# Performance work log

Hardware: AMD Instinct MI355X
Metric: run time of the kernel (lower is better)

## Reference

```python
import jax, jax.numpy as jnp
import numpy as np

N, E = 50000, 800000
IN_DIM, HID_DIM, OUT_DIM = 512, 256, 128


def setup_inputs() -> dict:
    key = jax.random.key(0)
    ks = jax.random.split(key, 10)
    x = jax.random.normal(ks[0], (N, IN_DIM), dtype=jnp.float32)
    edge_index = jax.random.randint(ks[1], (2, E), 0, N, dtype=jnp.int64)
    edge_weight = jax.random.uniform(ks[2], (E,), dtype=jnp.float32)
    # GCNConv weights (PyG stores weight as [in, out]; out = x @ W + b)
    def glorot(k, fan_in, fan_out):
        lim = np.sqrt(6.0 / (fan_in + fan_out)).astype(np.float32)
        return jax.random.uniform(k, (fan_in, fan_out), minval=-lim, maxval=lim, dtype=jnp.float32)
    W1 = glorot(ks[3], IN_DIM, HID_DIM)
    b1 = jnp.zeros((HID_DIM,), dtype=jnp.float32)
    W2 = glorot(ks[4], HID_DIM, OUT_DIM)
    b2 = jnp.zeros((OUT_DIM,), dtype=jnp.float32)
    Wp = glorot(ks[5], OUT_DIM, OUT_DIM)
    bp = jnp.zeros((OUT_DIM,), dtype=jnp.float32)
    return {"x": x, "edge_index": edge_index, "edge_weight": edge_weight,
            "W1": W1, "b1": b1, "W2": W2, "b2": b2, "Wp": Wp, "bp": bp}


def _gcn_norm(edge_index, edge_weight, n_nodes):
    # add self loops with weight 1.0 (PyG gcn_norm, fill_value=1.0)
    loops = jnp.arange(n_nodes, dtype=edge_index.dtype)
    row = jnp.concatenate([edge_index[0], loops])
    col = jnp.concatenate([edge_index[1], loops])
    w = jnp.concatenate([edge_weight, jnp.ones((n_nodes,), edge_weight.dtype)])
    deg = jax.ops.segment_sum(w, col, num_segments=n_nodes)  # [N]
    dinv = jnp.where(deg > 0, jax.lax.rsqrt(deg), 0.0)
    norm = dinv[row] * w * dinv[col]  # [E+N]
    return row, col, norm


def _gcn_conv(h, row, col, norm, W, b, n_nodes):
    h = h @ W                              # [N, out]
    msgs = h[row] * norm[:, None]          # gather + scale  [E+N, out]
    out = jax.ops.segment_sum(msgs, col, num_segments=n_nodes)  # scatter-add
    return out + b


def reference(x, edge_index, edge_weight, W1, b1, W2, b2, Wp, bp):
    n_nodes = x.shape[0]
    # eval mode: F.dropout(edge_weight, training=False) is identity
    row, col, norm = _gcn_norm(edge_index, edge_weight, n_nodes)
    h = jax.nn.relu(_gcn_conv(x, row, col, norm, W1, b1, n_nodes))
    # eval mode: F.dropout identity
    h = _gcn_conv(h, row, col, norm, W2, b2, n_nodes)
    return h @ Wp + bp
```

## Files before the change

kernel.cpp:

```cpp
#include <hip/hip_runtime.h>

#define IN_DIM 512
#define HID_DIM 256
#define OUT_DIM 128
#define BCAP 64

typedef unsigned short u16;
typedef __attribute__((ext_vector_type(8))) short bf16x8;
typedef __attribute__((ext_vector_type(4))) float f32x4;

__device__ inline u16 f2bf(float f) {
    unsigned u = __float_as_uint(f);
    return (u16)((u + 0x7FFFu + ((u >> 16) & 1u)) >> 16);
}
__device__ inline float bf2f(u16 u) {
    return __uint_as_float(((unsigned)u) << 16);
}

__device__ inline void gld_lds16(const void* g, void* l) {
    __builtin_amdgcn_global_load_lds((const __attribute__((address_space(1))) unsigned*)g,
                                     (__attribute__((address_space(3))) unsigned*)l, 16, 0, 0);
}


__global__ void bucket_fill_kernel(const int* __restrict__ row, const int* __restrict__ col,
                                   const float* __restrict__ w,
                                   int* __restrict__ cnt, int2* __restrict__ bucket, int E) {
    int e = blockIdx.x * blockDim.x + threadIdx.x;
    if (e >= E) return;
    int c = col[e];
    int slot = atomicAdd(&cnt[c], 1);
    if (slot < BCAP) {
        int2 v;
        v.x = row[e];
        v.y = __float_as_int(w[e]);
        bucket[(size_t)c * BCAP + slot] = v;
    }
}

__global__ void deg_dinv_kernel(const int2* __restrict__ bucket, const int* __restrict__ cnt,
                                float* __restrict__ dinv, int n) {
    int i = blockIdx.x * blockDim.x + threadIdx.x;
    if (i >= n) return;
    int c = min(cnt[i], BCAP);
    const int2* b = bucket + (size_t)i * BCAP;
    float s = 1.0f;
    for (int p = 0; p < c; ++p) s += __int_as_float(b[p].y);
    dinv[i] = (s > 0.0f) ? rsqrtf(s) : 0.0f;
}


__global__ void convert_x_kernel(const float* __restrict__ X, u16* __restrict__ Xb,
                                 int M, int Mpad) {
    long tid = (long)blockIdx.x * blockDim.x + threadIdx.x;
    long total = (long)Mpad * IN_DIM / 8;
    if (tid >= total) return;
    long base = tid * 8;
    int r = (int)(base / IN_DIM);
    ushort4 lo, hi;
    if (r < M) {
        float4 f0 = *(const float4*)(X + base);
        float4 f1 = *(const float4*)(X + base + 4);
        lo.x = f2bf(f0.x); lo.y = f2bf(f0.y); lo.z = f2bf(f0.z); lo.w = f2bf(f0.w);
        hi.x = f2bf(f1.x); hi.y = f2bf(f1.y); hi.z = f2bf(f1.z); hi.w = f2bf(f1.w);
    } else {
        lo.x = lo.y = lo.z = lo.w = 0;
        hi.x = hi.y = hi.z = hi.w = 0;
    }
    *(ushort4*)(Xb + base) = lo;
    *(ushort4*)(Xb + base + 4) = hi;
}

__global__ void transpose_bf_kernel(const float* __restrict__ W, u16* __restrict__ WT,
                                    int K, int Nc) {
    int idx = blockIdx.x * blockDim.x + threadIdx.x;
    if (idx >= K * Nc) return;
    int nrow = idx / K, k = idx - nrow * K;
    WT[idx] = f2bf(W[(size_t)k * Nc + nrow]);
}

__global__ void fuse_w2p_kernel(const float* __restrict__ W2, const float* __restrict__ Wp,
                                u16* __restrict__ W2pT) {
    int idx = blockIdx.x * blockDim.x + threadIdx.x;
    if (idx >= OUT_DIM * HID_DIM) return;
    int n = idx / HID_DIM, k = idx - n * HID_DIM;
    float s = 0.0f;
    for (int m = 0; m < OUT_DIM; ++m)
        s = fmaf(W2[(size_t)k * OUT_DIM + m], Wp[(size_t)m * OUT_DIM + n], s);
    W2pT[idx] = f2bf(s);
}

__global__ void fuse_bias2_kernel(const float* __restrict__ b2, const float* __restrict__ Wp,
                                  const float* __restrict__ bp, float* __restrict__ bias2) {
    int n = blockIdx.x * blockDim.x + threadIdx.x;
    if (n >= OUT_DIM) return;
    float s = bp[n];
    for (int m = 0; m < OUT_DIM; ++m)
        s = fmaf(b2[m], Wp[(size_t)m * OUT_DIM + n], s);
    bias2[n] = s;
}


#define TM 128
#define TN 128
#define TK 32

template <typename OutT>
__global__ __launch_bounds__(256)
void mfma_gemm_kernel(const u16* __restrict__ A, const u16* __restrict__ BT,
                      const float* __restrict__ bias, OutT* __restrict__ C,
                      int M, int Nc, int K) {
    __shared__ u16 As[TM * TK];
    __shared__ u16 Bs[TN * TK];
    const int tid = threadIdx.x;
    const int w = tid >> 6, l = tid & 63;
    const int wr = w >> 1, wc = w & 1;
    const long tile_m = (long)blockIdx.x * TM;
    const int tile_n = blockIdx.y * TN;

    const int r0 = w * 32 + (l >> 2);
    const int r1 = r0 + 16;
    const int c0 = l & 3;
    const long ga0 = (tile_m + r0) * (long)K + (long)((c0 ^ (r0 & 3)) * 8);
    const long ga1 = (tile_m + r1) * (long)K + (long)((c0 ^ (r1 & 3)) * 8);
    const long gb0 = (long)(tile_n + r0) * K + (long)((c0 ^ (r0 & 3)) * 8);
    const long gb1 = (long)(tile_n + r1) * K + (long)((c0 ^ (r1 & 3)) * 8);
    u16* ldsA0 = &As[(w * 2 + 0) * 512];
    u16* ldsA1 = &As[(w * 2 + 1) * 512];
    u16* ldsB0 = &Bs[(w * 2 + 0) * 512];
    u16* ldsB1 = &Bs[(w * 2 + 1) * 512];

    f32x4 acc[4][4] = {};
    const int lr = l & 15;
    const int kl = l >> 4;

    for (int k0 = 0; k0 < K; k0 += TK) {
        if (k0) __syncthreads();
        gld_lds16(A + ga0 + k0, ldsA0);
        gld_lds16(A + ga1 + k0, ldsA1);
        gld_lds16(BT + gb0 + k0, ldsB0);
        gld_lds16(BT + gb1 + k0, ldsB1);
        __syncthreads();

        bf16x8 af[4], bfv[4];
#pragma unroll
        for (int mi = 0; mi < 4; ++mi) {
            int rowi = wr * 64 + mi * 16 + lr;
            int byte = rowi * 64 + ((kl ^ (rowi & 3)) * 16);
            af[mi] = *(const bf16x8*)((const char*)As + byte);
        }
#pragma unroll
        for (int ni = 0; ni < 4; ++ni) {
            int rowi = wc * 64 + ni * 16 + lr;
            int byte = rowi * 64 + ((kl ^ (rowi & 3)) * 16);
            bfv[ni] = *(const bf16x8*)((const char*)Bs + byte);
        }
#pragma unroll
        for (int mi = 0; mi < 4; ++mi)
#pragma unroll
            for (int ni = 0; ni < 4; ++ni)
                acc[mi][ni] = __builtin_amdgcn_mfma_f32_16x16x32_bf16(af[mi], bfv[ni], acc[mi][ni], 0, 0, 0);
    }

    float bv[4];
#pragma unroll
    for (int ni = 0; ni < 4; ++ni)
        bv[ni] = bias ? bias[tile_n + wc * 64 + ni * 16 + lr] : 0.0f;
#pragma unroll
    for (int mi = 0; mi < 4; ++mi) {
#pragma unroll
        for (int reg = 0; reg < 4; ++reg) {
            long rowg = tile_m + wr * 64 + mi * 16 + kl * 4 + reg;
            if (rowg < M) {
#pragma unroll
                for (int ni = 0; ni < 4; ++ni) {
                    int colc = tile_n + wc * 64 + ni * 16 + lr;
                    float v = acc[mi][ni][reg] + bv[ni];
                    if constexpr (sizeof(OutT) == 2) C[rowg * Nc + colc] = f2bf(v);
                    else                             C[rowg * Nc + colc] = v;
                }
            }
        }
    }
}


template <int DIM, bool RELU, typename OutT>
__global__ __launch_bounds__(256)
void aggregate_kernel(const u16* __restrict__ t,
                      const int2* __restrict__ bucket,
                      const int* __restrict__ cnt,
                      const float* __restrict__ dinv,
                      const float* __restrict__ bias,
                      OutT* __restrict__ outp, int n) {
    constexpr int V = DIM / 64;
    const int wv = threadIdx.x >> 6;
    const int l = threadIdx.x & 63;
    const int node = blockIdx.x * 4 + wv;
    if (node >= n) return;
    const float dv = dinv[node];
    const float dv2 = dv * dv;
    float acc[V];
    if constexpr (V == 4) {
        ushort4 q = *(const ushort4*)(t + (size_t)node * DIM + l * 4);
        acc[0] = dv2 * bf2f(q.x); acc[1] = dv2 * bf2f(q.y);
        acc[2] = dv2 * bf2f(q.z); acc[3] = dv2 * bf2f(q.w);
    } else {
        ushort2 q = *(const ushort2*)(t + (size_t)node * DIM + l * 2);
        acc[0] = dv2 * bf2f(q.x); acc[1] = dv2 * bf2f(q.y);
    }
    const int e = min(cnt[node], BCAP);
    const int2* b = bucket + (size_t)node * BCAP;
    int p = 0;
    for (; p + 8 <= e; p += 8) {
        int2 ed[8];
        float wt[8];
#pragma unroll
        for (int j = 0; j < 8; ++j) ed[j] = b[p + j];
#pragma unroll
        for (int j = 0; j < 8; ++j) wt[j] = dv * __int_as_float(ed[j].y) * dinv[ed[j].x];
        if constexpr (V == 4) {
            ushort4 q[8];
#pragma unroll
            for (int j = 0; j < 8; ++j) q[j] = *(const ushort4*)(t + (size_t)ed[j].x * DIM + l * 4);
#pragma unroll
            for (int j = 0; j < 8; ++j) {
                acc[0] = fmaf(wt[j], bf2f(q[j].x), acc[0]);
                acc[1] = fmaf(wt[j], bf2f(q[j].y), acc[1]);
                acc[2] = fmaf(wt[j], bf2f(q[j].z), acc[2]);
                acc[3] = fmaf(wt[j], bf2f(q[j].w), acc[3]);
            }
        } else {
            ushort2 q[8];
#pragma unroll
            for (int j = 0; j < 8; ++j) q[j] = *(const ushort2*)(t + (size_t)ed[j].x * DIM + l * 2);
#pragma unroll
            for (int j = 0; j < 8; ++j) {
                acc[0] = fmaf(wt[j], bf2f(q[j].x), acc[0]);
                acc[1] = fmaf(wt[j], bf2f(q[j].y), acc[1]);
            }
        }
    }
    for (; p + 4 <= e; p += 4) {
        int2 ed[4];
        float wt[4];
#pragma unroll
        for (int j = 0; j < 4; ++j) ed[j] = b[p + j];
#pragma unroll
        for (int j = 0; j < 4; ++j) wt[j] = dv * __int_as_float(ed[j].y) * dinv[ed[j].x];
        if constexpr (V == 4) {
            ushort4 q[4];
#pragma unroll
            for (int j = 0; j < 4; ++j) q[j] = *(const ushort4*)(t + (size_t)ed[j].x * DIM + l * 4);
#pragma unroll
            for (int j = 0; j < 4; ++j) {
                acc[0] = fmaf(wt[j], bf2f(q[j].x), acc[0]);
                acc[1] = fmaf(wt[j], bf2f(q[j].y), acc[1]);
                acc[2] = fmaf(wt[j], bf2f(q[j].z), acc[2]);
                acc[3] = fmaf(wt[j], bf2f(q[j].w), acc[3]);
            }
        } else {
            ushort2 q[4];
#pragma unroll
            for (int j = 0; j < 4; ++j) q[j] = *(const ushort2*)(t + (size_t)ed[j].x * DIM + l * 2);
#pragma unroll
            for (int j = 0; j < 4; ++j) {
                acc[0] = fmaf(wt[j], bf2f(q[j].x), acc[0]);
                acc[1] = fmaf(wt[j], bf2f(q[j].y), acc[1]);
            }
        }
    }
    for (; p < e; ++p) {
        int2 e0 = b[p];
        float wgt = dv * __int_as_float(e0.y) * dinv[e0.x];
        if constexpr (V == 4) {
            ushort4 q = *(const ushort4*)(t + (size_t)e0.x * DIM + l * 4);
            acc[0] = fmaf(wgt, bf2f(q.x), acc[0]); acc[1] = fmaf(wgt, bf2f(q.y), acc[1]);
            acc[2] = fmaf(wgt, bf2f(q.z), acc[2]); acc[3] = fmaf(wgt, bf2f(q.w), acc[3]);
        } else {
            ushort2 q = *(const ushort2*)(t + (size_t)e0.x * DIM + l * 2);
            acc[0] = fmaf(wgt, bf2f(q.x), acc[0]); acc[1] = fmaf(wgt, bf2f(q.y), acc[1]);
        }
    }
#pragma unroll
    for (int j = 0; j < V; ++j) {
        float v = acc[j] + bias[l * V + j];
        if (RELU) v = fmaxf(v, 0.0f);
        acc[j] = v;
    }
    if constexpr (sizeof(OutT) == 2) {
        if constexpr (V == 4) {
            ushort4 st;
            st.x = f2bf(acc[0]); st.y = f2bf(acc[1]); st.z = f2bf(acc[2]); st.w = f2bf(acc[3]);
            *(ushort4*)((u16*)outp + (size_t)node * DIM + l * 4) = st;
        } else {
            ushort2 st;
            st.x = f2bf(acc[0]); st.y = f2bf(acc[1]);
            *(ushort2*)((u16*)outp + (size_t)node * DIM + l * 2) = st;
        }
    } else {
        if constexpr (V == 4) {
            float4 st = {acc[0], acc[1], acc[2], acc[3]};
            *(float4*)((float*)outp + (size_t)node * DIM + l * 4) = st;
        } else {
            float2 st = {acc[0], acc[1]};
            *(float2*)((float*)outp + (size_t)node * DIM + l * 2) = st;
        }
    }
}


extern "C" void kernel_launch(void* const* d_in, const int* in_sizes, int n_in,
                              void* d_out, int out_size, void* d_ws, size_t ws_size,
                              hipStream_t stream) {
    const float* x  = (const float*)d_in[0];
    const int*   ei = (const int*)d_in[1];
    const float* ew = (const float*)d_in[2];
    const float* W1 = (const float*)d_in[3];
    const float* b1 = (const float*)d_in[4];
    const float* W2 = (const float*)d_in[5];
    const float* b2 = (const float*)d_in[6];
    const float* Wp = (const float*)d_in[7];
    const float* bp = (const float*)d_in[8];
    float* out = (float*)d_out;

    const int E = in_sizes[2];
    const int N = in_sizes[0] / IN_DIM;
    const int Mpad = ((N + TM - 1) / TM) * TM;
    const int* row = ei;
    const int* col = ei + E;

    size_t off = 0;
    auto carve = [&](size_t bytes) -> void* {
        void* p = (char*)d_ws + off;
        off += (bytes + 255) & ~(size_t)255;
        return p;
    };
    float* dinv   = (float*)carve((size_t)N * 4);
    int*   cnt    = (int*)carve((size_t)N * 4);
    int2*  bucket = (int2*)carve((size_t)N * BCAP * 8);
    u16*   W1T    = (u16*)carve((size_t)HID_DIM * IN_DIM * 2);
    u16*   W2pT   = (u16*)carve((size_t)OUT_DIM * HID_DIM * 2);
    float* bias2  = (float*)carve((size_t)OUT_DIM * 4);
    u16*   bufA   = (u16*)carve((size_t)Mpad * IN_DIM * 2);
    u16*   bufB   = (u16*)carve((size_t)Mpad * HID_DIM * 2);

    u16* x_bf = bufA;
    u16* t1   = bufB;
    u16* a1   = bufA;
    u16* t3   = bufB;

    const int TB = 256;
    const int gN = (N + TB - 1) / TB;
    const int gE = (E + TB - 1) / TB;

    hipMemsetAsync(cnt, 0, (size_t)N * 4, stream);
    bucket_fill_kernel<<<gE, TB, 0, stream>>>(row, col, ew, cnt, bucket, E);
    deg_dinv_kernel<<<gN, TB, 0, stream>>>(bucket, cnt, dinv, N);

    convert_x_kernel<<<(int)(((long)Mpad * IN_DIM / 8 + TB - 1) / TB), TB, 0, stream>>>(x, x_bf, N, Mpad);
    transpose_bf_kernel<<<(IN_DIM * HID_DIM + TB - 1) / TB, TB, 0, stream>>>(W1, W1T, IN_DIM, HID_DIM);
    fuse_w2p_kernel<<<(OUT_DIM * HID_DIM + TB - 1) / TB, TB, 0, stream>>>(W2, Wp, W2pT);
    fuse_bias2_kernel<<<1, OUT_DIM, 0, stream>>>(b2, Wp, bp, bias2);

    const int gm = Mpad / TM;
    const int gagg = (N + 3) / 4;

    mfma_gemm_kernel<u16><<<dim3(gm, HID_DIM / TN), 256, 0, stream>>>(x_bf, W1T, nullptr, t1, Mpad, HID_DIM, IN_DIM);
    aggregate_kernel<HID_DIM, true, u16><<<gagg, 256, 0, stream>>>(t1, bucket, cnt, dinv, b1, a1, N);
    mfma_gemm_kernel<u16><<<dim3(gm, OUT_DIM / TN), 256, 0, stream>>>(a1, W2pT, nullptr, t3, Mpad, OUT_DIM, HID_DIM);
    aggregate_kernel<OUT_DIM, false, float><<<gagg, 256, 0, stream>>>(t3, bucket, cnt, dinv, bias2, out, N);
}
```

Measured before the change: 391.0 us.

## Fuse fp32-to-bf16 conversion of x into first GEMM and merge weight prep kernels

The first GEMM now reads fp32 x directly, converts it to bf16 in registers and writes it into LDS with the same XOR swizzle, masking rows past N. This removes the separate convert pass that wrote and re-read a padded bf16 copy of x. The three small weight and bias prep kernels are merged into one launch to cut launch overhead. The tradeoff is that the A-tile load goes from direct global-to-LDS copies to register-staged loads with conversion ALU work, which could slow the main loop.

Measured after the change: 370.3 us. 1.06x faster.

```diff
diff --git a/kernel.cpp b/kernel.cpp
--- a/kernel.cpp
+++ b/kernel.cpp
@@ -50,54 +50,37 @@
 }
 
 
-__global__ void convert_x_kernel(const float* __restrict__ X, u16* __restrict__ Xb,
-                                 int M, int Mpad) {
-    long tid = (long)blockIdx.x * blockDim.x + threadIdx.x;
-    long total = (long)Mpad * IN_DIM / 8;
-    if (tid >= total) return;
-    long base = tid * 8;
-    int r = (int)(base / IN_DIM);
-    ushort4 lo, hi;
-    if (r < M) {
-        float4 f0 = *(const float4*)(X + base);
-        float4 f1 = *(const float4*)(X + base + 4);
-        lo.x = f2bf(f0.x); lo.y = f2bf(f0.y); lo.z = f2bf(f0.z); lo.w = f2bf(f0.w);
-        hi.x = f2bf(f1.x); hi.y = f2bf(f1.y); hi.z = f2bf(f1.z); hi.w = f2bf(f1.w);
-    } else {
-        lo.x = lo.y = lo.z = lo.w = 0;
-        hi.x = hi.y = hi.z = hi.w = 0;
-    }
-    *(ushort4*)(Xb + base) = lo;
-    *(ushort4*)(Xb + base + 4) = hi;
-}
-
-__global__ void transpose_bf_kernel(const float* __restrict__ W, u16* __restrict__ WT,
-                                    int K, int Nc) {
-    int idx = blockIdx.x * blockDim.x + threadIdx.x;
-    if (idx >= K * Nc) return;
-    int nrow = idx / K, k = idx - nrow * K;
-    WT[idx] = f2bf(W[(size_t)k * Nc + nrow]);
-}
-
-__global__ void fuse_w2p_kernel(const float* __restrict__ W2, const float* __restrict__ Wp,
-                                u16* __restrict__ W2pT) {
-    int idx = blockIdx.x * blockDim.x + threadIdx.x;
-    if (idx >= OUT_DIM * HID_DIM) return;
-    int n = idx / HID_DIM, k = idx - n * HID_DIM;
-    float s = 0.0f;
-    for (int m = 0; m < OUT_DIM; ++m)
-        s = fmaf(W2[(size_t)k * OUT_DIM + m], Wp[(size_t)m * OUT_DIM + n], s);
-    W2pT[idx] = f2bf(s);
-}
-
-__global__ void fuse_bias2_kernel(const float* __restrict__ b2, const float* __restrict__ Wp,
-                                  const float* __restrict__ bp, float* __restrict__ bias2) {
-    int n = blockIdx.x * blockDim.x + threadIdx.x;
-    if (n >= OUT_DIM) return;
-    float s = bp[n];
-    for (int m = 0; m < OUT_DIM; ++m)
-        s = fmaf(b2[m], Wp[(size_t)m * OUT_DIM + n], s);
-    bias2[n] = s;
+__global__ __launch_bounds__(256)
+void weight_prep_kernel(const float* __restrict__ W1, u16* __restrict__ W1T,
+                        const float* __restrict__ W2, const float* __restrict__ Wp,
+                        const float* __restrict__ b2, const float* __restrict__ bp,
+                        u16* __restrict__ W2pT, float* __restrict__ bias2,
+                        int nW1, int nW2p) {
+    const int b = blockIdx.x;
+    const int tid = threadIdx.x;
+    if (b < nW1) {
+        int idx = b * 256 + tid;
+        if (idx >= IN_DIM * HID_DIM) return;
+        int nrow = idx / IN_DIM, k = idx - nrow * IN_DIM;
+        W1T[idx] = f2bf(W1[(size_t)k * HID_DIM + nrow]);
+        return;
+    }
+    if (b < nW1 + nW2p) {
+        int idx = (b - nW1) * 256 + tid;
+        if (idx >= OUT_DIM * HID_DIM) return;
+        int n = idx / HID_DIM, k = idx - n * HID_DIM;
+        float s = 0.0f;
+        for (int m = 0; m < OUT_DIM; ++m)
+            s = fmaf(W2[(size_t)k * OUT_DIM + m], Wp[(size_t)m * OUT_DIM + n], s);
+        W2pT[idx] = f2bf(s);
+        return;
+    }
+    if (tid < OUT_DIM) {
+        float s = bp[tid];
+        for (int m = 0; m < OUT_DIM; ++m)
+            s = fmaf(b2[m], Wp[(size_t)m * OUT_DIM + tid], s);
+        bias2[tid] = s;
+    }
 }
 
 
@@ -105,11 +88,11 @@
 #define TN 128
 #define TK 32
 
-template <typename OutT>
+template <typename AT, typename OutT>
 __global__ __launch_bounds__(256)
-void mfma_gemm_kernel(const u16* __restrict__ A, const u16* __restrict__ BT,
+void mfma_gemm_kernel(const AT* __restrict__ A, const u16* __restrict__ BT,
                       const float* __restrict__ bias, OutT* __restrict__ C,
-                      int M, int Nc, int K) {
+                      int Mreal, int Mpad, int Nc, int K) {
     __shared__ u16 As[TM * TK];
     __shared__ u16 Bs[TN * TK];
     const int tid = threadIdx.x;
@@ -121,14 +104,21 @@
     const int r0 = w * 32 + (l >> 2);
     const int r1 = r0 + 16;
     const int c0 = l & 3;
+    const long gb0 = (long)(tile_n + r0) * K + (long)((c0 ^ (r0 & 3)) * 8);
+    const long gb1 = (long)(tile_n + r1) * K + (long)((c0 ^ (r1 & 3)) * 8);
+    u16* ldsB0 = &Bs[(w * 2 + 0) * 512];
+    u16* ldsB1 = &Bs[(w * 2 + 1) * 512];
+
     const long ga0 = (tile_m + r0) * (long)K + (long)((c0 ^ (r0 & 3)) * 8);
     const long ga1 = (tile_m + r1) * (long)K + (long)((c0 ^ (r1 & 3)) * 8);
-    const long gb0 = (long)(tile_n + r0) * K + (long)((c0 ^ (r0 & 3)) * 8);
-    const long gb1 = (long)(tile_n + r1) * K + (long)((c0 ^ (r1 & 3)) * 8);
     u16* ldsA0 = &As[(w * 2 + 0) * 512];
     u16* ldsA1 = &As[(w * 2 + 1) * 512];
-    u16* ldsB0 = &Bs[(w * 2 + 0) * 512];
-    u16* ldsB1 = &Bs[(w * 2 + 1) * 512];
+
+    const int ci0 = tid, ci1 = tid + 256;
+    const int arow0 = ci0 >> 2, ach0 = ci0 & 3;
+    const int arow1 = ci1 >> 2, ach1 = ci1 & 3;
+    const int ag0 = (ach0 ^ (arow0 & 3)) * 8;
+    const int ag1 = (ach1 ^ (arow1 & 3)) * 8;
 
     f32x4 acc[4][4] = {};
     const int lr = l & 15;
@@ -136,8 +126,31 @@
 
     for (int k0 = 0; k0 < K; k0 += TK) {
         if (k0) __syncthreads();
-        gld_lds16(A + ga0 + k0, ldsA0);
-        gld_lds16(A + ga1 + k0, ldsA1);
+        if constexpr (sizeof(AT) == 4) {
+            float4 f0a = {0,0,0,0}, f0b = {0,0,0,0}, f1a = {0,0,0,0}, f1b = {0,0,0,0};
+            if (tile_m + arow0 < Mreal) {
+                const float* s0 = (const float*)A + (tile_m + arow0) * (long)K + k0 + ag0;
+                f0a = *(const float4*)s0; f0b = *(const float4*)(s0 + 4);
+            }
+            if (tile_m + arow1 < Mreal) {
+                const float* s1 = (const float*)A + (tile_m + arow1) * (long)K + k0 + ag1;
+                f1a = *(const float4*)s1; f1b = *(const float4*)(s1 + 4);
+            }
+            int4 w0, w1;
+            w0.x = f2bf(f0a.x) | ((unsigned)f2bf(f0a.y) << 16);
+            w0.y = f2bf(f0a.z) | ((unsigned)f2bf(f0a.w) << 16);
+            w0.z = f2bf(f0b.x) | ((unsigned)f2bf(f0b.y) << 16);
+            w0.w = f2bf(f0b.z) | ((unsigned)f2bf(f0b.w) << 16);
+            w1.x = f2bf(f1a.x) | ((unsigned)f2bf(f1a.y) << 16);
+            w1.y = f2bf(f1a.z) | ((unsigned)f2bf(f1a.w) << 16);
+            w1.z = f2bf(f1b.x) | ((unsigned)f2bf(f1b.y) << 16);
+            w1.w = f2bf(f1b.z) | ((unsigned)f2bf(f1b.w) << 16);
+            *(int4*)((char*)As + arow0 * 64 + ach0 * 16) = w0;
+            *(int4*)((char*)As + arow1 * 64 + ach1 * 16) = w1;
+        } else {
+            gld_lds16((const u16*)A + ga0 + k0, ldsA0);
+            gld_lds16((const u16*)A + ga1 + k0, ldsA1);
+        }
         gld_lds16(BT + gb0 + k0, ldsB0);
         gld_lds16(BT + gb1 + k0, ldsB1);
         __syncthreads();
@@ -171,7 +184,7 @@
 #pragma unroll
         for (int reg = 0; reg < 4; ++reg) {
             long rowg = tile_m + wr * 64 + mi * 16 + kl * 4 + reg;
-            if (rowg < M) {
+            if (rowg < Mpad) {
 #pragma unroll
                 for (int ni = 0; ni < 4; ++ni) {
                     int colc = tile_n + wc * 64 + ni * 16 + lr;
@@ -342,32 +355,30 @@
     u16*   W1T    = (u16*)carve((size_t)HID_DIM * IN_DIM * 2);
     u16*   W2pT   = (u16*)carve((size_t)OUT_DIM * HID_DIM * 2);
     float* bias2  = (float*)carve((size_t)OUT_DIM * 4);
-    u16*   bufA   = (u16*)carve((size_t)Mpad * IN_DIM * 2);
+    u16*   bufA   = (u16*)carve((size_t)Mpad * HID_DIM * 2);
     u16*   bufB   = (u16*)carve((size_t)Mpad * HID_DIM * 2);
 
-    u16* x_bf = bufA;
-    u16* t1   = bufB;
-    u16* a1   = bufA;
-    u16* t3   = bufB;
+    u16* t1 = bufB;
+    u16* a1 = bufA;
+    u16* t3 = bufB;
 
     const int TB = 256;
     const int gN = (N + TB - 1) / TB;
     const int gE = (E + TB - 1) / TB;
 
+    const int nW1  = (IN_DIM * HID_DIM + TB - 1) / TB;
+    const int nW2p = (OUT_DIM * HID_DIM + TB - 1) / TB;
+
     hipMemsetAsync(cnt, 0, (size_t)N * 4, stream);
     bucket_fill_kernel<<<gE, TB, 0, stream>>>(row, col, ew, cnt, bucket, E);
+    weight_prep_kernel<<<nW1 + nW2p + 1, TB, 0, stream>>>(W1, W1T, W2, Wp, b2, bp, W2pT, bias2, nW1, nW2p);
     deg_dinv_kernel<<<gN, TB, 0, stream>>>(bucket, cnt, dinv, N);
-
-    convert_x_kernel<<<(int)(((long)Mpad * IN_DIM / 8 + TB - 1) / TB), TB, 0, stream>>>(x, x_bf, N, Mpad);
-    transpose_bf_kernel<<<(IN_DIM * HID_DIM + TB - 1) / TB, TB, 0, stream>>>(W1, W1T, IN_DIM, HID_DIM);
-    fuse_w2p_kernel<<<(OUT_DIM * HID_DIM + TB - 1) / TB, TB, 0, stream>>>(W2, Wp, W2pT);
-    fuse_bias2_kernel<<<1, OUT_DIM, 0, stream>>>(b2, Wp, bp, bias2);
 
     const int gm = Mpad / TM;
     const int gagg = (N + 3) / 4;
 
-    mfma_gemm_kernel<u16><<<dim3(gm, HID_DIM / TN), 256, 0, stream>>>(x_bf, W1T, nullptr, t1, Mpad, HID_DIM, IN_DIM);
+    mfma_gemm_kernel<float, u16><<<dim3(gm, HID_DIM / TN), 256, 0, stream>>>(x, W1T, nullptr, t1, N, Mpad, HID_DIM, IN_DIM);
     aggregate_kernel<HID_DIM, true, u16><<<gagg, 256, 0, stream>>>(t1, bucket, cnt, dinv, b1, a1, N);
-    mfma_gemm_kernel<u16><<<dim3(gm, OUT_DIM / TN), 256, 0, stream>>>(a1, W2pT, nullptr, t3, Mpad, OUT_DIM, HID_DIM);
+    mfma_gemm_kernel<u16, u16><<<dim3(gm, OUT_DIM / TN), 256, 0, stream>>>(a1, W2pT, nullptr, t3, N, Mpad, OUT_DIM, HID_DIM);
     aggregate_kernel<OUT_DIM, false, float><<<gagg, 256, 0, stream>>>(t3, bucket, cnt, dinv, bias2, out, N);
 }
```
